# Kernel optimization log

Hardware: AMD Instinct MI355X
Metric: run time of the kernel (lower is better)

The kernel has to match this reference:

```python
import jax, jax.numpy as jnp
import numpy as np

EMBED = 1024
HEADS = 16
HEAD_DIM = EMBED // HEADS


def setup_inputs() -> dict:
    key = jax.random.key(0)
    ks = jax.random.split(key, 11)
    B, S = 4, 2048
    scale = 1.0 / np.sqrt(EMBED)
    inp = {
        "query": jax.random.normal(ks[0], (B, S, EMBED), jnp.float32),
        "key": jax.random.normal(ks[1], (B, S, EMBED), jnp.float32),
        "value": jax.random.normal(ks[2], (B, S, EMBED), jnp.float32),
        "Wq": jax.random.normal(ks[3], (EMBED, EMBED), jnp.float32) * scale,
        "bq": jnp.zeros((EMBED,), jnp.float32),
        "Wk": jax.random.normal(ks[4], (EMBED, EMBED), jnp.float32) * scale,
        "bk": jnp.zeros((EMBED,), jnp.float32),
        "Wv": jax.random.normal(ks[5], (EMBED, EMBED), jnp.float32) * scale,
        "bv": jnp.zeros((EMBED,), jnp.float32),
        "Wo": jax.random.normal(ks[6], (EMBED, EMBED), jnp.float32) * scale,
        "bo": jnp.zeros((EMBED,), jnp.float32),
    }
    return inp


def reference(query, key, value, Wq, bq, Wk, bk, Wv, bv, Wo, bo):
    B, Sq, _ = query.shape
    Sk = key.shape[1]
    # projections, split heads: (B, H, S, D)
    def proj(x, W, b, S):
        return (x @ W.T + b).reshape(B, S, HEADS, HEAD_DIM).transpose(0, 2, 1, 3)
    q = proj(query, Wq, bq, Sq)
    k = proj(key, Wk, bk, Sk)
    v = proj(value, Wv, bv, Sk)
    energy = jnp.einsum("bhqd,bhkd->bhqk", q, k) / np.sqrt(HEAD_DIM)
    attn = jax.nn.softmax(energy, axis=-1)
    out = jnp.einsum("bhqk,bhkd->bhqd", attn, v)
    out = out.transpose(0, 2, 1, 3).reshape(B, Sq, EMBED)
    return out @ Wo.T + bo
```

## Files before the change

### kernel.cpp

```cpp
#include <hip/hip_runtime.h>
#include <hip/hip_bf16.h>

typedef __bf16 bf16x8 __attribute__((ext_vector_type(8)));
typedef float f32x4 __attribute__((ext_vector_type(4)));
typedef float f32x16 __attribute__((ext_vector_type(16)));
typedef unsigned short ushortx8 __attribute__((ext_vector_type(8)));
typedef unsigned short ushortx4 __attribute__((ext_vector_type(4)));

#define B_ 4
#define S_ 2048
#define E_ 1024
#define H_ 16
#define D_ 64

static __device__ __forceinline__ unsigned short f2bf(float f) {
    union { float f; unsigned u; } v; v.f = f;
    unsigned r = v.u + 0x7FFFu + ((v.u >> 16) & 1u);
    return (unsigned short)(r >> 16);
}

static __device__ __forceinline__ unsigned cvtpk(float lo, float hi) {
    unsigned r;
    asm("v_cvt_pk_bf16_f32 %0, %1, %2" : "=v"(r) : "v"(lo), "v"(hi));
    return r;
}

static __device__ __forceinline__ void gload16(const void* g, void* l) {
    __builtin_amdgcn_global_load_lds(
        (const __attribute__((address_space(1))) unsigned int*)g,
        (__attribute__((address_space(3))) unsigned int*)l, 16, 0, 0);
}

static __device__ __forceinline__ void store_out(float* p, float v) { *p = v; }
static __device__ __forceinline__ void store_out(unsigned short* p, float v) { *p = f2bf(v); }

static __device__ __forceinline__ void cast_one(const float* s, unsigned short* d, int i) {
    float4 f = ((const float4*)s)[i];
    ushortx4 u;
    u[0] = f2bf(f.x); u[1] = f2bf(f.y); u[2] = f2bf(f.z); u[3] = f2bf(f.w);
    ((ushortx4*)d)[i] = u;
}

__global__ void cast3_f32_bf16(const float* __restrict__ s0, unsigned short* __restrict__ d0,
                               const float* __restrict__ s1, unsigned short* __restrict__ d1,
                               const float* __restrict__ s2, unsigned short* __restrict__ d2,
                               int n4) {
    int stride = gridDim.x * blockDim.x;
    for (int i = blockIdx.x * blockDim.x + threadIdx.x; i < 3 * n4; i += stride) {
        int which = i / n4, j = i - which * n4;
        const float* s = which == 0 ? s0 : (which == 1 ? s1 : s2);
        unsigned short* d = which == 0 ? d0 : (which == 1 ? d1 : d2);
        cast_one(s, d, j);
    }
}

__global__ void cast4_f32_bf16(const float* __restrict__ s0, unsigned short* __restrict__ d0,
                               const float* __restrict__ s1, unsigned short* __restrict__ d1,
                               const float* __restrict__ s2, unsigned short* __restrict__ d2,
                               const float* __restrict__ s3, unsigned short* __restrict__ d3,
                               int n4) {
    int stride = gridDim.x * blockDim.x;
    for (int i = blockIdx.x * blockDim.x + threadIdx.x; i < 4 * n4; i += stride) {
        int which = i / n4, j = i - which * n4;
        const float* s = which == 0 ? s0 : (which == 1 ? s1 : (which == 2 ? s2 : s3));
        unsigned short* d = which == 0 ? d0 : (which == 1 ? d1 : (which == 2 ? d2 : d3));
        cast_one(s, d, j);
    }
}

template <typename OutT>
static __device__ __forceinline__ void gemm_body(
    const unsigned short* __restrict__ A,
    const unsigned short* __restrict__ Bt,
    const float* __restrict__ bias,
    OutT* __restrict__ C,
    int N, int K, float scale, char* lds) {
    char* ldsA = lds;
    char* ldsB = lds + 16384;
    const int t = threadIdx.x;
    const int w = t >> 6, l = t & 63, lo = l & 15, hi = l >> 4;
    const int wr = w >> 1, wc = w & 1;
    const int m0 = blockIdx.x * 128, n0 = blockIdx.y * 128;
    const char* Ab = (const char*)A;
    const char* Bb = (const char*)Bt;
    const size_t ldab = (size_t)K * 2;

    f32x4 acc[4][4];
#pragma unroll
    for (int m = 0; m < 4; ++m)
#pragma unroll
        for (int n = 0; n < 4; ++n) acc[m][n] = (f32x4){0.f, 0.f, 0.f, 0.f};

    const int nk = K >> 6;
    for (int kt = 0; kt < nk; ++kt) {
        const int k0b = kt * 128;
        __syncthreads();
#pragma unroll
        for (int r = 0; r < 4; ++r) {
            int p = (r * 256 + t) * 16;
            int row = p >> 7, x = p & 127;
            int sw = (row & 7) << 4;
            gload16(Ab + (size_t)(m0 + row) * ldab + k0b + (x ^ sw), ldsA + p);
            gload16(Bb + (size_t)(n0 + row) * ldab + k0b + (x ^ sw), ldsB + p);
        }
        asm volatile("s_waitcnt vmcnt(0)" ::: "memory");
        __syncthreads();
#pragma unroll
        for (int kk = 0; kk < 2; ++kk) {
            bf16x8 af[4], bfr[4];
#pragma unroll
            for (int m = 0; m < 4; ++m) {
                int row = wr * 64 + m * 16 + lo;
                af[m] = *(const bf16x8*)(ldsA + row * 128 +
                                         ((kk * 64 + hi * 16) ^ ((row & 7) << 4)));
            }
#pragma unroll
            for (int n = 0; n < 4; ++n) {
                int row = wc * 64 + n * 16 + lo;
                bfr[n] = *(const bf16x8*)(ldsB + row * 128 +
                                          ((kk * 64 + hi * 16) ^ ((row & 7) << 4)));
            }
#pragma unroll
            for (int m = 0; m < 4; ++m)
#pragma unroll
                for (int n = 0; n < 4; ++n)
                    acc[m][n] = __builtin_amdgcn_mfma_f32_16x16x32_bf16(
                        af[m], bfr[n], acc[m][n], 0, 0, 0);
        }
    }
#pragma unroll
    for (int n = 0; n < 4; ++n) {
        int col = n0 + wc * 64 + n * 16 + lo;
        float bv = bias[col];
#pragma unroll
        for (int m = 0; m < 4; ++m)
#pragma unroll
            for (int r = 0; r < 4; ++r) {
                int row = m0 + wr * 64 + m * 16 + hi * 4 + r;
                float val = (acc[m][n][r] + bv) * scale;
                store_out(C + (size_t)row * N + col, val);
            }
    }
}

__global__ __launch_bounds__(256) void gemm_qkv(
    const unsigned short* __restrict__ A0, const unsigned short* __restrict__ A1,
    const unsigned short* __restrict__ A2,
    const unsigned short* __restrict__ W0, const unsigned short* __restrict__ W1,
    const unsigned short* __restrict__ W2,
    const float* __restrict__ b0, const float* __restrict__ b1,
    const float* __restrict__ b2,
    unsigned short* __restrict__ C0, unsigned short* __restrict__ C1,
    unsigned short* __restrict__ C2, float scale0) {
    __shared__ char lds[32768];
    const int z = blockIdx.z;
    const unsigned short* A = z == 0 ? A0 : (z == 1 ? A1 : A2);
    const unsigned short* W = z == 0 ? W0 : (z == 1 ? W1 : W2);
    const float* bias = z == 0 ? b0 : (z == 1 ? b1 : b2);
    unsigned short* C = z == 0 ? C0 : (z == 1 ? C1 : C2);
    float scale = z == 0 ? scale0 : 1.f;
    gemm_body<unsigned short>(A, W, bias, C, 1024, 1024, scale, lds);
}

__global__ __launch_bounds__(256) void gemm_out(
    const unsigned short* __restrict__ A,
    const unsigned short* __restrict__ Bt,
    const float* __restrict__ bias,
    float* __restrict__ C) {
    __shared__ char lds[32768];
    gemm_body<float>(A, Bt, bias, C, 1024, 1024, 1.f, lds);
}

__global__ __launch_bounds__(256) void attn_fwd(
    const unsigned short* __restrict__ Qg,
    const unsigned short* __restrict__ Kg,
    const unsigned short* __restrict__ Vg,
    unsigned short* __restrict__ Og) {
    __shared__ char lds[32768];

    const int t = threadIdx.x;
    const int w = t >> 6, l = t & 63;
    const int lo5 = l & 31, hi5 = l >> 5;
    const int bid = blockIdx.x;
    const int remap = (bid & 7) * 128 + (bid >> 3);
    const int bh = remap >> 4, qt = remap & 15;
    const int b = bh >> 4, h = bh & 15;

    const char* Qb = (const char*)(Qg + ((size_t)b * S_ + qt * 128) * E_ + h * 64);
    const char* Kb = (const char*)(Kg + (size_t)b * S_ * E_ + h * 64);
    const char* Vb = (const char*)(Vg + (size_t)b * S_ * E_ + h * 64);

    size_t koff[2]; int kdst[2];
#pragma unroll
    for (int r = 0; r < 2; ++r) {
        int p = (r * 256 + t) * 16;
        int row = p >> 7, x = p & 127;
        koff[r] = (size_t)row * 2048 + (x ^ ((row & 7) << 4));
        kdst[r] = p;
    }
    const int kvp = t >> 3, oct = t & 7;
    ushortx8 vr0, vr1;

#define STAGE_K(bufi, tile) do {                                 \
        const char* Ks_ = Kb + (size_t)(tile) * 131072;          \
        char* kb_ = lds + ((bufi) << 13);                        \
        gload16(Ks_ + koff[0], kb_ + kdst[0]);                   \
        gload16(Ks_ + koff[1], kb_ + kdst[1]);                   \
    } while (0)

#define VLOAD(tile) do {                                         \
        const char* vs_ = Vb + (size_t)(tile) * 131072 +         \
                          (size_t)(2 * kvp) * 2048 + oct * 16;   \
        vr0 = *(const ushortx8*)(vs_);                           \
        vr1 = *(const ushortx8*)(vs_ + 2048);                    \
    } while (0)

#define VWRITE(bufi) do {                                        \
        char* vt_ = lds + 16384 + ((bufi) << 13);                \
        _Pragma("unroll")                                        \
        for (int s_ = 0; s_ < 8; ++s_) {                         \
            int i_ = (s_ + oct) & 7;                             \
            int d_ = oct * 8 + i_;                               \
            unsigned val_ = (unsigned)vr0[i_] |                  \
                            ((unsigned)vr1[i_] << 16);           \
            *(unsigned*)(vt_ + d_ * 128 +                        \
                         ((kvp * 4) ^ (i_ << 4))) = val_;        \
        }                                                        \
    } while (0)

    VLOAD(0);
    STAGE_K(0, 0);

    bf16x8 qf[4];
#pragma unroll
    for (int st = 0; st < 4; ++st)
        qf[st] = *(const bf16x8*)(Qb + (size_t)(w * 32 + lo5) * 2048 +
                                  st * 32 + hi5 * 16);

    bf16x8 ones;
#pragma unroll
    for (int j = 0; j < 8; ++j) ones[j] = (__bf16)1.0f;
    f32x16 zf;
#pragma unroll
    for (int r = 0; r < 16; ++r) zf[r] = 0.f;

    f32x16 o0, o1, osum;
#pragma unroll
    for (int r = 0; r < 16; ++r) { o0[r] = 0.f; o1[r] = 0.f; osum[r] = 0.f; }

    VWRITE(0);
    asm volatile("s_waitcnt vmcnt(0)" ::: "memory");
    __syncthreads();

    for (int tile = 0; tile < S_ / 64; ++tile) {
        const int buf = tile & 1;
        const bool last = (tile == S_ / 64 - 1);
        if (!last) {
            VLOAD(tile + 1);
            STAGE_K(buf ^ 1, tile + 1);
        }

        const char* kb_ = lds + (buf << 13);
        const char* vtb = lds + 16384 + (buf << 13);
        const int sw5 = (lo5 & 7) << 4;

        f32x16 s0, s1;
        __builtin_amdgcn_s_setprio(1);
        {
            bf16x8 kf0 = *(const bf16x8*)(kb_ + lo5 * 128 + ((hi5 * 16) ^ sw5));
            bf16x8 kf1 = *(const bf16x8*)(kb_ + (lo5 + 32) * 128 + ((hi5 * 16) ^ sw5));
            s0 = __builtin_amdgcn_mfma_f32_32x32x16_bf16(kf0, qf[0], zf, 0, 0, 0);
            s1 = __builtin_amdgcn_mfma_f32_32x32x16_bf16(kf1, qf[0], zf, 0, 0, 0);
        }
#pragma unroll
        for (int st = 1; st < 4; ++st) {
            bf16x8 kf0 = *(const bf16x8*)(kb_ + lo5 * 128 +
                                          ((st * 32 + hi5 * 16) ^ sw5));
            bf16x8 kf1 = *(const bf16x8*)(kb_ + (lo5 + 32) * 128 +
                                          ((st * 32 + hi5 * 16) ^ sw5));
            s0 = __builtin_amdgcn_mfma_f32_32x32x16_bf16(kf0, qf[st], s0, 0, 0, 0);
            s1 = __builtin_amdgcn_mfma_f32_32x32x16_bf16(kf1, qf[st], s1, 0, 0, 0);
        }
        __builtin_amdgcn_s_setprio(0);

        unsigned c[2][4][2];
#pragma unroll
        for (int i = 0; i < 4; ++i)
#pragma unroll
            for (int u = 0; u < 2; ++u) {
                float pa0 = __builtin_amdgcn_exp2f(s0[4 * i + 2 * u]);
                float pb0 = __builtin_amdgcn_exp2f(s0[4 * i + 2 * u + 1]);
                float pa1 = __builtin_amdgcn_exp2f(s1[4 * i + 2 * u]);
                float pb1 = __builtin_amdgcn_exp2f(s1[4 * i + 2 * u + 1]);
                c[0][i][u] = cvtpk(pa0, pb0);
                c[1][i][u] = cvtpk(pa1, pb1);
            }

        bf16x8 pf[4];
#pragma unroll
        for (int st = 0; st < 4; ++st) {
            const int g = st >> 1, p2 = (st & 1) * 2;
            auto r0 = __builtin_amdgcn_permlane32_swap(c[g][p2][0], c[g][p2 + 1][0],
                                                       false, false);
            auto r1 = __builtin_amdgcn_permlane32_swap(c[g][p2][1], c[g][p2 + 1][1],
                                                       false, false);
            union { unsigned u[4]; bf16x8 v; } fu;
            fu.u[0] = r0[0]; fu.u[1] = r1[0]; fu.u[2] = r0[1]; fu.u[3] = r1[1];
            pf[st] = fu.v;
        }

        __builtin_amdgcn_s_setprio(1);
#pragma unroll
        for (int st = 0; st < 4; ++st) {
            bf16x8 vf0 = *(const bf16x8*)(vtb + lo5 * 128 +
                                          ((st * 32 + hi5 * 16) ^ sw5));
            bf16x8 vf1 = *(const bf16x8*)(vtb + (lo5 + 32) * 128 +
                                          ((st * 32 + hi5 * 16) ^ sw5));
            o0 = __builtin_amdgcn_mfma_f32_32x32x16_bf16(vf0, pf[st], o0, 0, 0, 0);
            o1 = __builtin_amdgcn_mfma_f32_32x32x16_bf16(vf1, pf[st], o1, 0, 0, 0);
            osum = __builtin_amdgcn_mfma_f32_32x32x16_bf16(ones, pf[st], osum, 0, 0, 0);
        }
        __builtin_amdgcn_s_setprio(0);

        if (!last) {
            VWRITE(buf ^ 1);
            __syncthreads();
        }
    }
#undef STAGE_K
#undef VLOAD
#undef VWRITE

    float inv = 1.f / osum[0];
    unsigned short* orow = Og + ((size_t)b * S_ + qt * 128 + w * 32 + lo5) * E_ + h * 64;
#pragma unroll
    for (int rq = 0; rq < 4; ++rq) {
        ushortx4 u0, u1;
#pragma unroll
        for (int j = 0; j < 4; ++j) {
            u0[j] = f2bf(o0[4 * rq + j] * inv);
            u1[j] = f2bf(o1[4 * rq + j] * inv);
        }
        *(ushortx4*)(orow + 8 * rq + 4 * hi5) = u0;
        *(ushortx4*)(orow + 8 * rq + 4 * hi5 + 32) = u1;
    }
}

extern "C" void kernel_launch(void* const* d_in, const int* in_sizes, int n_in,
                              void* d_out, int out_size, void* d_ws, size_t ws_size,
                              hipStream_t stream) {
    const float* q  = (const float*)d_in[0];
    const float* k  = (const float*)d_in[1];
    const float* v  = (const float*)d_in[2];
    const float* Wq = (const float*)d_in[3];
    const float* bq = (const float*)d_in[4];
    const float* Wk = (const float*)d_in[5];
    const float* bk = (const float*)d_in[6];
    const float* Wv = (const float*)d_in[7];
    const float* bv = (const float*)d_in[8];
    const float* Wo = (const float*)d_in[9];
    const float* bo = (const float*)d_in[10];

    unsigned short* ws = (unsigned short*)d_ws;
    const size_t TE = (size_t)B_ * S_ * E_;
    const size_t WE = (size_t)E_ * E_;
    unsigned short* qb  = ws;
    unsigned short* kb  = qb + TE;
    unsigned short* vb  = kb + TE;
    unsigned short* Wqb = vb + TE;
    unsigned short* Wkb = Wqb + WE;
    unsigned short* Wvb = Wkb + WE;
    unsigned short* Wob = Wvb + WE;
    unsigned short* Qp  = Wob + WE;
    unsigned short* Kp  = Qp + TE;
    unsigned short* Vp  = Kp + TE;

    cast3_f32_bf16<<<2048, 256, 0, stream>>>(q, qb, k, kb, v, vb, (int)(TE / 4));
    cast4_f32_bf16<<<1024, 256, 0, stream>>>(Wq, Wqb, Wk, Wkb, Wv, Wvb, Wo, Wob,
                                             (int)(WE / 4));

    const float qscale = 0.125f * 1.44269504088896f;
    gemm_qkv<<<dim3(64, 8, 3), 256, 0, stream>>>(qb, kb, vb, Wqb, Wkb, Wvb,
                                                 bq, bk, bv, Qp, Kp, Vp, qscale);

    attn_fwd<<<1024, 256, 0, stream>>>(Qp, Kp, Vp, qb);

    gemm_out<<<dim3(64, 8), 256, 0, stream>>>(qb, Wob, bo, (float*)d_out);
}
```

Measured before the change: 242.6 us.

## Fuse fp32-to-bf16 activation cast into QKV projection GEMM loads

Drops the separate cast kernel for query/key/value. The QKV GEMM now reads fp32 activations directly with register loads, converts them to bf16 with v_cvt_pk_bf16_f32 and writes them into swizzled LDS, while the weight tile still arrives via global_load_lds. This removes one full write and re-read of three bf16 activation tensors. In exchange the GEMM moves twice the activation bytes each K step and waits synchronously on the register loads, with no overlap of fetch and compute.

Measured after the change: 272.3 us. +12.3%, slower.

```diff
diff --git a/kernel.cpp b/kernel.cpp
--- a/kernel.cpp
+++ b/kernel.cpp
@@ -4,6 +4,7 @@
 typedef __bf16 bf16x8 __attribute__((ext_vector_type(8)));
 typedef float f32x4 __attribute__((ext_vector_type(4)));
 typedef float f32x16 __attribute__((ext_vector_type(16)));
+typedef unsigned int u32x4 __attribute__((ext_vector_type(4)));
 typedef unsigned short ushortx8 __attribute__((ext_vector_type(8)));
 typedef unsigned short ushortx4 __attribute__((ext_vector_type(4)));
 
@@ -39,19 +40,6 @@
     ushortx4 u;
     u[0] = f2bf(f.x); u[1] = f2bf(f.y); u[2] = f2bf(f.z); u[3] = f2bf(f.w);
     ((ushortx4*)d)[i] = u;
-}
-
-__global__ void cast3_f32_bf16(const float* __restrict__ s0, unsigned short* __restrict__ d0,
-                               const float* __restrict__ s1, unsigned short* __restrict__ d1,
-                               const float* __restrict__ s2, unsigned short* __restrict__ d2,
-                               int n4) {
-    int stride = gridDim.x * blockDim.x;
-    for (int i = blockIdx.x * blockDim.x + threadIdx.x; i < 3 * n4; i += stride) {
-        int which = i / n4, j = i - which * n4;
-        const float* s = which == 0 ? s0 : (which == 1 ? s1 : s2);
-        unsigned short* d = which == 0 ? d0 : (which == 1 ? d1 : d2);
-        cast_one(s, d, j);
-    }
 }
 
 __global__ void cast4_f32_bf16(const float* __restrict__ s0, unsigned short* __restrict__ d0,
@@ -65,6 +53,98 @@
         const float* s = which == 0 ? s0 : (which == 1 ? s1 : (which == 2 ? s2 : s3));
         unsigned short* d = which == 0 ? d0 : (which == 1 ? d1 : (which == 2 ? d2 : d3));
         cast_one(s, d, j);
+    }
+}
+
+static __device__ __forceinline__ void gemm_body_f32a(
+    const float* __restrict__ A,
+    const unsigned short* __restrict__ Bt,
+    const float* __restrict__ bias,
+    unsigned short* __restrict__ C,
+    int N, int K, float scale, char* lds) {
+    char* ldsA = lds;
+    char* ldsB = lds + 16384;
+    const int t = threadIdx.x;
+    const int w = t >> 6, l = t & 63, lo = l & 15, hi = l >> 4;
+    const int wr = w >> 1, wc = w & 1;
+    const int m0 = blockIdx.x * 128, n0 = blockIdx.y * 128;
+    const char* Ab = (const char*)A;
+    const char* Bb = (const char*)Bt;
+    const size_t ldab = (size_t)K * 2;
+    const size_t ldaf = (size_t)K * 4;
+
+    const int arow = t >> 1, ahalf = t & 1;
+    const char* Asrc = Ab + (size_t)(m0 + arow) * ldaf + ahalf * 128;
+    const int aswz = (arow & 7) << 4;
+    char* Adst = ldsA + arow * 128;
+
+    f32x4 acc[4][4];
+#pragma unroll
+    for (int m = 0; m < 4; ++m)
+#pragma unroll
+        for (int n = 0; n < 4; ++n) acc[m][n] = (f32x4){0.f, 0.f, 0.f, 0.f};
+
+    const int nk = K >> 6;
+    for (int kt = 0; kt < nk; ++kt) {
+        const int k0b = kt * 128;
+        __syncthreads();
+#pragma unroll
+        for (int r = 0; r < 4; ++r) {
+            int p = (r * 256 + t) * 16;
+            int row = p >> 7, x = p & 127;
+            int sw = (row & 7) << 4;
+            gload16(Bb + (size_t)(n0 + row) * ldab + k0b + (x ^ sw), ldsB + p);
+        }
+        float4 av[8];
+#pragma unroll
+        for (int j = 0; j < 8; ++j)
+            av[j] = *(const float4*)(Asrc + (size_t)kt * 256 + j * 16);
+        asm volatile("s_waitcnt vmcnt(0)" ::: "memory");
+#pragma unroll
+        for (int j2 = 0; j2 < 4; ++j2) {
+            u32x4 q;
+            q[0] = cvtpk(av[2 * j2].x, av[2 * j2].y);
+            q[1] = cvtpk(av[2 * j2].z, av[2 * j2].w);
+            q[2] = cvtpk(av[2 * j2 + 1].x, av[2 * j2 + 1].y);
+            q[3] = cvtpk(av[2 * j2 + 1].z, av[2 * j2 + 1].w);
+            *(u32x4*)(Adst + ((ahalf * 64 + j2 * 16) ^ aswz)) = q;
+        }
+        __syncthreads();
+#pragma unroll
+        for (int kk = 0; kk < 2; ++kk) {
+            bf16x8 af[4], bfr[4];
+#pragma unroll
+            for (int m = 0; m < 4; ++m) {
+                int row = wr * 64 + m * 16 + lo;
+                af[m] = *(const bf16x8*)(ldsA + row * 128 +
+                                         ((kk * 64 + hi * 16) ^ ((row & 7) << 4)));
+            }
+#pragma unroll
+            for (int n = 0; n < 4; ++n) {
+                int row = wc * 64 + n * 16 + lo;
+                bfr[n] = *(const bf16x8*)(ldsB + row * 128 +
+                                          ((kk * 64 + hi * 16) ^ ((row & 7) << 4)));
+            }
+#pragma unroll
+            for (int m = 0; m < 4; ++m)
+#pragma unroll
+                for (int n = 0; n < 4; ++n)
+                    acc[m][n] = __builtin_amdgcn_mfma_f32_16x16x32_bf16(
+                        af[m], bfr[n], acc[m][n], 0, 0, 0);
+        }
+    }
+#pragma unroll
+    for (int n = 0; n < 4; ++n) {
+        int col = n0 + wc * 64 + n * 16 + lo;
+        float bv = bias[col];
+#pragma unroll
+        for (int m = 0; m < 4; ++m)
+#pragma unroll
+            for (int r = 0; r < 4; ++r) {
+                int row = m0 + wr * 64 + m * 16 + hi * 4 + r;
+                float val = (acc[m][n][r] + bv) * scale;
+                store_out(C + (size_t)row * N + col, val);
+            }
     }
 }
 
@@ -144,8 +224,8 @@
 }
 
 __global__ __launch_bounds__(256) void gemm_qkv(
-    const unsigned short* __restrict__ A0, const unsigned short* __restrict__ A1,
-    const unsigned short* __restrict__ A2,
+    const float* __restrict__ A0, const float* __restrict__ A1,
+    const float* __restrict__ A2,
     const unsigned short* __restrict__ W0, const unsigned short* __restrict__ W1,
     const unsigned short* __restrict__ W2,
     const float* __restrict__ b0, const float* __restrict__ b1,
@@ -154,12 +234,12 @@
     unsigned short* __restrict__ C2, float scale0) {
     __shared__ char lds[32768];
     const int z = blockIdx.z;
-    const unsigned short* A = z == 0 ? A0 : (z == 1 ? A1 : A2);
+    const float* A = z == 0 ? A0 : (z == 1 ? A1 : A2);
     const unsigned short* W = z == 0 ? W0 : (z == 1 ? W1 : W2);
     const float* bias = z == 0 ? b0 : (z == 1 ? b1 : b2);
     unsigned short* C = z == 0 ? C0 : (z == 1 ? C1 : C2);
     float scale = z == 0 ? scale0 : 1.f;
-    gemm_body<unsigned short>(A, W, bias, C, 1024, 1024, scale, lds);
+    gemm_body_f32a(A, W, bias, C, 1024, 1024, scale, lds);
 }
 
 __global__ __launch_bounds__(256) void gemm_out(
@@ -365,9 +445,7 @@
     const size_t TE = (size_t)B_ * S_ * E_;
     const size_t WE = (size_t)E_ * E_;
     unsigned short* qb  = ws;
-    unsigned short* kb  = qb + TE;
-    unsigned short* vb  = kb + TE;
-    unsigned short* Wqb = vb + TE;
+    unsigned short* Wqb = qb + TE;
     unsigned short* Wkb = Wqb + WE;
     unsigned short* Wvb = Wkb + WE;
     unsigned short* Wob = Wvb + WE;
@@ -375,12 +453,11 @@
     unsigned short* Kp  = Qp + TE;
     unsigned short* Vp  = Kp + TE;
 
-    cast3_f32_bf16<<<2048, 256, 0, stream>>>(q, qb, k, kb, v, vb, (int)(TE / 4));
     cast4_f32_bf16<<<1024, 256, 0, stream>>>(Wq, Wqb, Wk, Wkb, Wv, Wvb, Wo, Wob,
                                              (int)(WE / 4));
 
     const float qscale = 0.125f * 1.44269504088896f;
-    gemm_qkv<<<dim3(64, 8, 3), 256, 0, stream>>>(qb, kb, vb, Wqb, Wkb, Wvb,
+    gemm_qkv<<<dim3(64, 8, 3), 256, 0, stream>>>(q, k, v, Wqb, Wkb, Wvb,
                                                  bq, bk, bv, Qp, Kp, Vp, qscale);
 
     attn_fwd<<<1024, 256, 0, stream>>>(Qp, Kp, Vp, qb);
```
